# Kernel tuning notes

Hardware: AMD Instinct MI355X
Metric: run time of the kernel (lower is better)

The kernel has to match this reference:

```python
import jax, jax.numpy as jnp
import numpy as np

VOCAB = 1000
SEQ = 80
EMB = 128
UNITS = 128
BATCH = 4096


def setup_inputs() -> dict:
    key = jax.random.key(0)
    ks = jax.random.split(key, 10)
    s = 0.05
    return {
        "inputs": jax.random.randint(ks[0], (BATCH, SEQ), 0, VOCAB, dtype=jnp.int32),
        "emb": jax.random.normal(ks[1], (VOCAB, EMB), jnp.float32) * s,
        "Wx0": jax.random.normal(ks[2], (EMB, UNITS), jnp.float32) * s,
        "Wh0": jax.random.normal(ks[3], (UNITS, UNITS), jnp.float32) * s,
        "b0": jnp.zeros((UNITS,), jnp.float32),
        "Wx1": jax.random.normal(ks[4], (UNITS, UNITS), jnp.float32) * s,
        "Wh1": jax.random.normal(ks[5], (UNITS, UNITS), jnp.float32) * s,
        "b1": jnp.zeros((UNITS,), jnp.float32),
        "Wout": jax.random.normal(ks[6], (UNITS, 1), jnp.float32) * s,
        "bout": jnp.zeros((1,), jnp.float32),
    }


def reference(inputs, emb, Wx0, Wh0, b0, Wx1, Wh1, b1, Wout, bout):
    # Embedding lookup: [B, S, EMB]
    x = emb[inputs]
    B = x.shape[0]
    h0_init = jnp.zeros((B, UNITS), x.dtype)
    h1_init = jnp.zeros((B, UNITS), x.dtype)

    # Precompute input projections for both cells' input terms where possible.
    # Layer 0 input term depends only on x: [S, B, UNITS]
    x_t = jnp.einsum('bse,eu->sbu', x, Wx0) + b0

    def step(carry, xw):
        h0, h1 = carry
        # SimpleRNNCell 0: h = tanh(x@Wx + h@Wh + b)  (dropout off: inference)
        h0 = jnp.tanh(xw + h0 @ Wh0)
        # SimpleRNNCell 1 stacked on layer-0 output
        h1 = jnp.tanh(h0 @ Wx1 + h1 @ Wh1 + b1)
        return (h0, h1), None

    (h0, h1), _ = jax.lax.scan(step, (h0_init, h1_init), x_t)
    logits = h1 @ Wout + bout          # [B, 1]
    prob = jax.nn.sigmoid(logits)
    return prob
```

## Files before the change

### kernel.cpp

```cpp
#include <hip/hip_runtime.h>
#include <hip/hip_bf16.h>

#define VOCAB 1000
#define SEQ   80
#define EMB   128
#define UNITS 128
#define BATCH 4096

typedef short bf16x8 __attribute__((ext_vector_type(8)));
typedef float f32x4  __attribute__((ext_vector_type(4)));
typedef float f32x2  __attribute__((ext_vector_type(2)));

__device__ inline unsigned short f2bf(float x) {
    union { float f; unsigned int u; } c; c.f = x;
    unsigned int r = c.u + 0x7fffu + ((c.u >> 16) & 1u);
    return (unsigned short)(r >> 16);
}
__device__ inline float bf2f(unsigned short h) {
    union { unsigned int u; float f; } c; c.u = ((unsigned int)h) << 16;
    return c.f;
}
__device__ inline f32x2 th2(f32x2 x) {
    f32x2 x2 = x * x;
    f32x2 p = __builtin_elementwise_fma(x2, (f32x2)(0.13333334f), (f32x2)(-0.33333334f));
    p = __builtin_elementwise_fma(x2, p, (f32x2)(1.0f));
    return x * p;
}
__device__ inline unsigned int cvt_pk_bf16(float lo, float hi) {
    unsigned int r;
    asm("v_cvt_pk_bf16_f32 %0, %1, %2" : "=v"(r) : "v"(lo), "v"(hi));
    return r;
}
__device__ inline void lds_sync() {
    asm volatile("s_waitcnt lgkmcnt(0)\n\ts_barrier" ::: "memory");
}

__device__ __host__ inline int sigma(int u) {
    const int m = u >> 4, g = (u >> 2) & 3, r = u & 3;
    return ((m & 3) << 5) | (g << 3) | ((m >> 2) << 2) | r;
}

__global__ void __launch_bounds__(256)
prep_kernel(const float* __restrict__ emb, const float* __restrict__ Wx0,
            const float* __restrict__ b0, const float* __restrict__ Wh0,
            const float* __restrict__ Wx1, const float* __restrict__ Wh1,
            float* __restrict__ embW, unsigned short* __restrict__ WT)
{
    const int blk = blockIdx.x;
    const int tid = threadIdx.x;
    if (blk < VOCAB) {
        __shared__ float erow[EMB];
        __shared__ float part[EMB];
        const int u = tid & 127, half = tid >> 7;
        if (tid < EMB) erow[tid] = emb[blk * EMB + tid];
        __syncthreads();
        const int p = sigma(u);
        float s = half ? 0.f : b0[p];
        const int e0 = half * 64;
        #pragma unroll 8
        for (int e = e0; e < e0 + 64; ++e)
            s = fmaf(erow[e], Wx0[e * UNITS + p], s);
        if (half) part[u] = s;
        __syncthreads();
        if (!half) embW[blk * UNITS + u] = s + part[u];
    } else {
        const int mat = blk - VOCAB;
        const float* src = (mat == 0) ? Wh0 : (mat == 1) ? Wx1 : Wh1;
        for (int j = tid; j < UNITS * UNITS; j += 256) {
            const int row = j >> 7, k = j & 127;
            WT[mat * 16384 + j] = f2bf(src[k * UNITS + sigma(row)]);
        }
    }
}

__global__ void __launch_bounds__(512, 2)
rnn_kernel(const int* __restrict__ inputs, const float* __restrict__ embW,
           const unsigned short* __restrict__ WT, const float* __restrict__ b1,
           const float* __restrict__ Wout, const float* __restrict__ bout,
           float* __restrict__ out)
{
    __shared__ int idx_lds[SEQ * 16];
    __shared__ __align__(16) unsigned char h0buf[2][16 * 256];
    __shared__ __align__(16) unsigned char h1buf[2][16 * 256];

    const int tid  = threadIdx.x;
    const int lane = tid & 63;
    const int wid  = tid >> 6;
    const int w    = wid & 3;
    const int R    = blockIdx.x * 16;

    for (int j = tid; j < SEQ * 16; j += 512) {
        const int i = j / SEQ, t = j - i * SEQ;
        idx_lds[t * 16 + i] = inputs[(R + i) * SEQ + t];
    }
    for (int j = tid; j < 1024; j += 512) {
        ((unsigned int*)h0buf[0])[j] = 0u;
        ((unsigned int*)h1buf[0])[j] = 0u;
    }
    __syncthreads();

    const int lrow = lane & 15;
    const int lgrp = lane >> 4;
    const int lk8  = lgrp * 8;

    const int bswz   = (lrow & 7) << 4;
    const int rdbase = lrow * 256;
    const int woff   = (rdbase + w * 64 + lgrp * 16) ^ bswz;
    int cur = 0;

    if (wid < 4) {
        bf16x8 aW0[2][4];
        #pragma unroll
        for (int i = 0; i < 2; ++i)
            #pragma unroll
            for (int kk = 0; kk < 4; ++kk)
                aW0[i][kk] = *reinterpret_cast<const bf16x8*>(
                    WT + 0 * 16384 + ((w + 4 * i) * 16 + lrow) * 128 + kk * 32 + lk8);

        float4 xw_n[2];
        {
            const int row = idx_lds[lrow];
            xw_n[0] = *reinterpret_cast<const float4*>(embW + row * 128 + w * 16 + lgrp * 4);
            xw_n[1] = *reinterpret_cast<const float4*>(embW + row * 128 + (w + 4) * 16 + lgrp * 4);
        }

        __builtin_amdgcn_s_setprio(1);
        for (int t = 0; t <= SEQ; ++t) {
            const float4 xw0 = xw_n[0], xw1 = xw_n[1];
            const int tn   = (t < SEQ - 1) ? t + 1 : SEQ - 1;
            const int rown = idx_lds[tn * 16 + lrow];
            xw_n[0] = *reinterpret_cast<const float4*>(embW + rown * 128 + w * 16 + lgrp * 4);
            xw_n[1] = *reinterpret_cast<const float4*>(embW + rown * 128 + (w + 4) * 16 + lgrp * 4);

            bf16x8 f0[4];
            #pragma unroll
            for (int kk = 0; kk < 4; ++kk) {
                const int off = (rdbase + kk * 64 + lgrp * 16) ^ bswz;
                f0[kk] = *reinterpret_cast<const bf16x8*>(h0buf[cur] + off);
            }
            f32x4 acc0[2];
            acc0[0][0] = xw0.x; acc0[0][1] = xw0.y; acc0[0][2] = xw0.z; acc0[0][3] = xw0.w;
            acc0[1][0] = xw1.x; acc0[1][1] = xw1.y; acc0[1][2] = xw1.z; acc0[1][3] = xw1.w;

            #pragma unroll
            for (int kk = 0; kk < 4; ++kk) {
                acc0[0] = __builtin_amdgcn_mfma_f32_16x16x32_bf16(aW0[0][kk], f0[kk], acc0[0], 0, 0, 0);
                acc0[1] = __builtin_amdgcn_mfma_f32_16x16x32_bf16(aW0[1][kk], f0[kk], acc0[1], 0, 0, 0);
            }

            const f32x2 p0 = th2(f32x2{acc0[0][0], acc0[0][1]});
            const f32x2 p1 = th2(f32x2{acc0[0][2], acc0[0][3]});
            const f32x2 p2 = th2(f32x2{acc0[1][0], acc0[1][1]});
            const f32x2 p3 = th2(f32x2{acc0[1][2], acc0[1][3]});
            int4 q;
            q.x = (int)cvt_pk_bf16(p0.x, p0.y);
            q.y = (int)cvt_pk_bf16(p1.x, p1.y);
            q.z = (int)cvt_pk_bf16(p2.x, p2.y);
            q.w = (int)cvt_pk_bf16(p3.x, p3.y);
            *reinterpret_cast<int4*>(h0buf[cur ^ 1] + woff) = q;

            lds_sync();
            cur ^= 1;
        }
        __builtin_amdgcn_s_setprio(0);
    } else {
        bf16x8 aWx[2][4], aWh[2][4];
        #pragma unroll
        for (int i = 0; i < 2; ++i)
            #pragma unroll
            for (int kk = 0; kk < 4; ++kk) {
                const int rb = ((w + 4 * i) * 16 + lrow) * 128 + kk * 32 + lk8;
                aWx[i][kk] = *reinterpret_cast<const bf16x8*>(WT + 1 * 16384 + rb);
                aWh[i][kk] = *reinterpret_cast<const bf16x8*>(WT + 2 * 16384 + rb);
            }
        float4 b1v[2];
        b1v[0] = *reinterpret_cast<const float4*>(b1 + w * 32 + lgrp * 8 + 0);
        b1v[1] = *reinterpret_cast<const float4*>(b1 + w * 32 + lgrp * 8 + 4);

        for (int t = 0; t <= SEQ; ++t) {
            bf16x8 f0[4], f1[4];
            #pragma unroll
            for (int kk = 0; kk < 4; ++kk) {
                const int off = (rdbase + kk * 64 + lgrp * 16) ^ bswz;
                f0[kk] = *reinterpret_cast<const bf16x8*>(h0buf[cur] + off);
                f1[kk] = *reinterpret_cast<const bf16x8*>(h1buf[cur] + off);
            }

            f32x4 accA[2], accB[2];
            accA[0][0] = b1v[0].x; accA[0][1] = b1v[0].y; accA[0][2] = b1v[0].z; accA[0][3] = b1v[0].w;
            accA[1][0] = b1v[1].x; accA[1][1] = b1v[1].y; accA[1][2] = b1v[1].z; accA[1][3] = b1v[1].w;
            accB[0][0] = 0.f; accB[0][1] = 0.f; accB[0][2] = 0.f; accB[0][3] = 0.f;
            accB[1][0] = 0.f; accB[1][1] = 0.f; accB[1][2] = 0.f; accB[1][3] = 0.f;

            #pragma unroll
            for (int kk = 0; kk < 4; ++kk) {
                accA[0] = __builtin_amdgcn_mfma_f32_16x16x32_bf16(aWx[0][kk], f0[kk], accA[0], 0, 0, 0);
                accA[1] = __builtin_amdgcn_mfma_f32_16x16x32_bf16(aWx[1][kk], f0[kk], accA[1], 0, 0, 0);
                accB[0] = __builtin_amdgcn_mfma_f32_16x16x32_bf16(aWh[0][kk], f1[kk], accB[0], 0, 0, 0);
                accB[1] = __builtin_amdgcn_mfma_f32_16x16x32_bf16(aWh[1][kk], f1[kk], accB[1], 0, 0, 0);
            }

            const f32x2 p0 = th2(f32x2{accA[0][0] + accB[0][0], accA[0][1] + accB[0][1]});
            const f32x2 p1 = th2(f32x2{accA[0][2] + accB[0][2], accA[0][3] + accB[0][3]});
            const f32x2 p2 = th2(f32x2{accA[1][0] + accB[1][0], accA[1][1] + accB[1][1]});
            const f32x2 p3 = th2(f32x2{accA[1][2] + accB[1][2], accA[1][3] + accB[1][3]});
            int4 q;
            q.x = (int)cvt_pk_bf16(p0.x, p0.y);
            q.y = (int)cvt_pk_bf16(p1.x, p1.y);
            q.z = (int)cvt_pk_bf16(p2.x, p2.y);
            q.w = (int)cvt_pk_bf16(p3.x, p3.y);
            *reinterpret_cast<int4*>(h1buf[cur ^ 1] + woff) = q;

            lds_sync();
            cur ^= 1;
        }
    }

    if (wid == 0) {
        const int b = lrow;
        float s = 0.f;
        #pragma unroll
        for (int uu = 0; uu < 32; ++uu) {
            const int u   = lgrp * 32 + uu;
            const int off = (b * 256 + u * 2) ^ ((b & 7) << 4);
            s += bf2f(*reinterpret_cast<const unsigned short*>(h1buf[cur] + off)) * Wout[u];
        }
        s += __shfl_xor(s, 16);
        s += __shfl_xor(s, 32);
        if (lane < 16) {
            const float z = s + bout[0];
            const float e = __builtin_amdgcn_exp2f(-z * 1.4426950408889634f);
            out[R + b] = __builtin_amdgcn_rcpf(1.f + e);
        }
    }
}

extern "C" void kernel_launch(void* const* d_in, const int* in_sizes, int n_in,
                              void* d_out, int out_size, void* d_ws, size_t ws_size,
                              hipStream_t stream)
{
    (void)in_sizes; (void)n_in; (void)out_size; (void)ws_size;
    const int*   inputs = (const int*)  d_in[0];
    const float* emb    = (const float*)d_in[1];
    const float* Wx0    = (const float*)d_in[2];
    const float* Wh0    = (const float*)d_in[3];
    const float* b0     = (const float*)d_in[4];
    const float* Wx1    = (const float*)d_in[5];
    const float* Wh1    = (const float*)d_in[6];
    const float* b1     = (const float*)d_in[7];
    const float* Wout   = (const float*)d_in[8];
    const float* bout   = (const float*)d_in[9];
    float* out = (float*)d_out;

    float*          embW = (float*)d_ws;
    unsigned short* WT   = (unsigned short*)((char*)d_ws + 524288);

    prep_kernel<<<VOCAB + 3, 256, 0, stream>>>(emb, Wx0, b0, Wh0, Wx1, Wh1, embW, WT);
    rnn_kernel<<<BATCH / 16, 512, 0, stream>>>(inputs, embW, WT, b1, Wout, bout, out);
}
```

Before: 54.96 us.

## Replicate layer-0 recurrence per wave to keep h0 in registers

Each layer-0 wave now holds all eight Wh0 tiles and recomputes the full 128-unit h0 for its batch rows, feeding the result straight back through registers instead of reading it from LDS. The embedding input is added after the MFMAs instead of being used as the accumulator seed. Only the wave's own slice is still written to LDS for layer 1. Layer-1 waves reuse their own previous h1 slice from registers, and the raised wave priority moves from layer 0 to layer 1. This trades four times the layer-0 MFMA work, more registers and an unprefetched embedding load for less LDS traffic on the critical recurrence.

```diff
diff --git a/kernel.cpp b/kernel.cpp
--- a/kernel.cpp
+++ b/kernel.cpp
@@ -86,7 +86,6 @@
     const int tid  = threadIdx.x;
     const int lane = tid & 63;
     const int wid  = tid >> 6;
-    const int w    = wid & 3;
     const int R    = blockIdx.x * 16;
 
     for (int j = tid; j < SEQ * 16; j += 512) {
@@ -105,65 +104,66 @@
 
     const int bswz   = (lrow & 7) << 4;
     const int rdbase = lrow * 256;
-    const int woff   = (rdbase + w * 64 + lgrp * 16) ^ bswz;
     int cur = 0;
 
     if (wid < 4) {
-        bf16x8 aW0[2][4];
-        #pragma unroll
-        for (int i = 0; i < 2; ++i)
+        const int w = wid;
+        bf16x8 aW0[8][4];
+        #pragma unroll
+        for (int m = 0; m < 8; ++m)
             #pragma unroll
             for (int kk = 0; kk < 4; ++kk)
-                aW0[i][kk] = *reinterpret_cast<const bf16x8*>(
-                    WT + 0 * 16384 + ((w + 4 * i) * 16 + lrow) * 128 + kk * 32 + lk8);
-
-        float4 xw_n[2];
-        {
-            const int row = idx_lds[lrow];
-            xw_n[0] = *reinterpret_cast<const float4*>(embW + row * 128 + w * 16 + lgrp * 4);
-            xw_n[1] = *reinterpret_cast<const float4*>(embW + row * 128 + (w + 4) * 16 + lgrp * 4);
-        }
-
-        __builtin_amdgcn_s_setprio(1);
+                aW0[m][kk] = *reinterpret_cast<const bf16x8*>(
+                    WT + (m * 16 + lrow) * 128 + kk * 32 + lk8);
+
+        bf16x8 fb[4];
+        #pragma unroll
+        for (int kk = 0; kk < 4; ++kk) fb[kk] = (bf16x8)(short)0;
+
+        const int woff = (rdbase + w * 64 + lgrp * 16) ^ bswz;
+
         for (int t = 0; t <= SEQ; ++t) {
-            const float4 xw0 = xw_n[0], xw1 = xw_n[1];
-            const int tn   = (t < SEQ - 1) ? t + 1 : SEQ - 1;
-            const int rown = idx_lds[tn * 16 + lrow];
-            xw_n[0] = *reinterpret_cast<const float4*>(embW + rown * 128 + w * 16 + lgrp * 4);
-            xw_n[1] = *reinterpret_cast<const float4*>(embW + rown * 128 + (w + 4) * 16 + lgrp * 4);
-
-            bf16x8 f0[4];
-            #pragma unroll
-            for (int kk = 0; kk < 4; ++kk) {
-                const int off = (rdbase + kk * 64 + lgrp * 16) ^ bswz;
-                f0[kk] = *reinterpret_cast<const bf16x8*>(h0buf[cur] + off);
-            }
-            f32x4 acc0[2];
-            acc0[0][0] = xw0.x; acc0[0][1] = xw0.y; acc0[0][2] = xw0.z; acc0[0][3] = xw0.w;
-            acc0[1][0] = xw1.x; acc0[1][1] = xw1.y; acc0[1][2] = xw1.z; acc0[1][3] = xw1.w;
-
-            #pragma unroll
-            for (int kk = 0; kk < 4; ++kk) {
-                acc0[0] = __builtin_amdgcn_mfma_f32_16x16x32_bf16(aW0[0][kk], f0[kk], acc0[0], 0, 0, 0);
-                acc0[1] = __builtin_amdgcn_mfma_f32_16x16x32_bf16(aW0[1][kk], f0[kk], acc0[1], 0, 0, 0);
-            }
-
-            const f32x2 p0 = th2(f32x2{acc0[0][0], acc0[0][1]});
-            const f32x2 p1 = th2(f32x2{acc0[0][2], acc0[0][3]});
-            const f32x2 p2 = th2(f32x2{acc0[1][0], acc0[1][1]});
-            const f32x2 p3 = th2(f32x2{acc0[1][2], acc0[1][3]});
-            int4 q;
-            q.x = (int)cvt_pk_bf16(p0.x, p0.y);
-            q.y = (int)cvt_pk_bf16(p1.x, p1.y);
-            q.z = (int)cvt_pk_bf16(p2.x, p2.y);
-            q.w = (int)cvt_pk_bf16(p3.x, p3.y);
-            *reinterpret_cast<int4*>(h0buf[cur ^ 1] + woff) = q;
+            const int tc   = (t < SEQ) ? t : SEQ - 1;
+            const int rowC = idx_lds[tc * 16 + lrow];
+            float4 xw[8];
+            #pragma unroll
+            for (int m = 0; m < 8; ++m)
+                xw[m] = *reinterpret_cast<const float4*>(
+                    embW + rowC * 128 + m * 16 + lgrp * 4);
+
+            f32x4 acc[8];
+            #pragma unroll
+            for (int m = 0; m < 8; ++m)
+                acc[m] = __builtin_amdgcn_mfma_f32_16x16x32_bf16(
+                    aW0[m][0], fb[0], (f32x4){0.f, 0.f, 0.f, 0.f}, 0, 0, 0);
+            #pragma unroll
+            for (int kk = 1; kk < 4; ++kk)
+                #pragma unroll
+                for (int m = 0; m < 8; ++m)
+                    acc[m] = __builtin_amdgcn_mfma_f32_16x16x32_bf16(
+                        aW0[m][kk], fb[kk], acc[m], 0, 0, 0);
+
+            #pragma unroll
+            for (int kk = 0; kk < 4; ++kk) {
+                const f32x2 p0 = th2(f32x2{acc[kk][0] + xw[kk].x, acc[kk][1] + xw[kk].y});
+                const f32x2 p1 = th2(f32x2{acc[kk][2] + xw[kk].z, acc[kk][3] + xw[kk].w});
+                const f32x2 p2 = th2(f32x2{acc[kk + 4][0] + xw[kk + 4].x, acc[kk + 4][1] + xw[kk + 4].y});
+                const f32x2 p3 = th2(f32x2{acc[kk + 4][2] + xw[kk + 4].z, acc[kk + 4][3] + xw[kk + 4].w});
+                int4 q;
+                q.x = (int)cvt_pk_bf16(p0.x, p0.y);
+                q.y = (int)cvt_pk_bf16(p1.x, p1.y);
+                q.z = (int)cvt_pk_bf16(p2.x, p2.y);
+                q.w = (int)cvt_pk_bf16(p3.x, p3.y);
+                if (kk == w)
+                    *reinterpret_cast<int4*>(h0buf[cur ^ 1] + woff) = q;
+                fb[kk] = __builtin_bit_cast(bf16x8, q);
+            }
 
             lds_sync();
             cur ^= 1;
         }
-        __builtin_amdgcn_s_setprio(0);
     } else {
+        const int w = wid - 4;
         bf16x8 aWx[2][4], aWh[2][4];
         #pragma unroll
         for (int i = 0; i < 2; ++i)
@@ -177,13 +177,22 @@
         b1v[0] = *reinterpret_cast<const float4*>(b1 + w * 32 + lgrp * 8 + 0);
         b1v[1] = *reinterpret_cast<const float4*>(b1 + w * 32 + lgrp * 8 + 4);
 
+        bf16x8 fbk1 = (bf16x8)(short)0;
+        const int woff = (rdbase + w * 64 + lgrp * 16) ^ bswz;
+
+        __builtin_amdgcn_s_setprio(1);
         for (int t = 0; t <= SEQ; ++t) {
             bf16x8 f0[4], f1[4];
             #pragma unroll
             for (int kk = 0; kk < 4; ++kk) {
                 const int off = (rdbase + kk * 64 + lgrp * 16) ^ bswz;
                 f0[kk] = *reinterpret_cast<const bf16x8*>(h0buf[cur] + off);
-                f1[kk] = *reinterpret_cast<const bf16x8*>(h1buf[cur] + off);
+            }
+            #pragma unroll
+            for (int kk = 0; kk < 4; ++kk) {
+                if (kk == w) f1[kk] = fbk1;
+                else f1[kk] = *reinterpret_cast<const bf16x8*>(
+                        h1buf[cur] + ((rdbase + kk * 64 + lgrp * 16) ^ bswz));
             }
 
             f32x4 accA[2], accB[2];
@@ -210,10 +219,12 @@
             q.z = (int)cvt_pk_bf16(p2.x, p2.y);
             q.w = (int)cvt_pk_bf16(p3.x, p3.y);
             *reinterpret_cast<int4*>(h1buf[cur ^ 1] + woff) = q;
+            fbk1 = __builtin_bit_cast(bf16x8, q);
 
             lds_sync();
             cur ^= 1;
         }
+        __builtin_amdgcn_s_setprio(0);
     }
 
     if (wid == 0) {
```

After: 129.0 us. 135% more time.

## Move layer-1 input projection to layer-0 waves and deepen wave pipeline

Applied to the files above, without the earlier changes.

The layer-1 input product h0@Wx1 plus bias is now computed by the layer-0 waves right after their own step and staged through a new double-buffered fp32 LDS buffer. The layer-1 waves then only do the recurrent h1@Wh1 product, which shortens their critical path per step and balances MFMA work between the two wave groups. The pipeline grows by one step and adds LDS traffic and footprint (16KB zbuf), which could lower occupancy. It also changes which waves set high priority, since only the layer-0 recurrence is prioritized.

```diff
diff --git a/kernel.cpp b/kernel.cpp
--- a/kernel.cpp
+++ b/kernel.cpp
@@ -82,6 +82,7 @@
     __shared__ int idx_lds[SEQ * 16];
     __shared__ __align__(16) unsigned char h0buf[2][16 * 256];
     __shared__ __align__(16) unsigned char h1buf[2][16 * 256];
+    __shared__ __align__(16) unsigned char zbuf[2][8192];
 
     const int tid  = threadIdx.x;
     const int lane = tid & 63;
@@ -93,7 +94,7 @@
         const int i = j / SEQ, t = j - i * SEQ;
         idx_lds[t * 16 + i] = inputs[(R + i) * SEQ + t];
     }
-    for (int j = tid; j < 1024; j += 512) {
+    for (int j = tid; j < 2048; j += 512) {
         ((unsigned int*)h0buf[0])[j] = 0u;
         ((unsigned int*)h1buf[0])[j] = 0u;
     }
@@ -106,16 +107,22 @@
     const int bswz   = (lrow & 7) << 4;
     const int rdbase = lrow * 256;
     const int woff   = (rdbase + w * 64 + lgrp * 16) ^ bswz;
-    int cur = 0;
+    const int zo0    = w * 2048 + lane * 16;
+    const int zo1    = w * 2048 + 1024 + lane * 16;
 
     if (wid < 4) {
-        bf16x8 aW0[2][4];
+        bf16x8 aW0[2][4], aWx[2][4];
         #pragma unroll
         for (int i = 0; i < 2; ++i)
             #pragma unroll
-            for (int kk = 0; kk < 4; ++kk)
-                aW0[i][kk] = *reinterpret_cast<const bf16x8*>(
-                    WT + 0 * 16384 + ((w + 4 * i) * 16 + lrow) * 128 + kk * 32 + lk8);
+            for (int kk = 0; kk < 4; ++kk) {
+                const int rb = ((w + 4 * i) * 16 + lrow) * 128 + kk * 32 + lk8;
+                aW0[i][kk] = *reinterpret_cast<const bf16x8*>(WT + 0 * 16384 + rb);
+                aWx[i][kk] = *reinterpret_cast<const bf16x8*>(WT + 1 * 16384 + rb);
+            }
+        float4 b1v[2];
+        b1v[0] = *reinterpret_cast<const float4*>(b1 + w * 32 + lgrp * 8 + 0);
+        b1v[1] = *reinterpret_cast<const float4*>(b1 + w * 32 + lgrp * 8 + 4);
 
         float4 xw_n[2];
         {
@@ -124,95 +131,95 @@
             xw_n[1] = *reinterpret_cast<const float4*>(embW + row * 128 + (w + 4) * 16 + lgrp * 4);
         }
 
-        __builtin_amdgcn_s_setprio(1);
-        for (int t = 0; t <= SEQ; ++t) {
-            const float4 xw0 = xw_n[0], xw1 = xw_n[1];
-            const int tn   = (t < SEQ - 1) ? t + 1 : SEQ - 1;
-            const int rown = idx_lds[tn * 16 + lrow];
-            xw_n[0] = *reinterpret_cast<const float4*>(embW + rown * 128 + w * 16 + lgrp * 4);
-            xw_n[1] = *reinterpret_cast<const float4*>(embW + rown * 128 + (w + 4) * 16 + lgrp * 4);
-
+        for (int t = 0; t <= SEQ + 1; ++t) {
             bf16x8 f0[4];
-            #pragma unroll
-            for (int kk = 0; kk < 4; ++kk) {
-                const int off = (rdbase + kk * 64 + lgrp * 16) ^ bswz;
-                f0[kk] = *reinterpret_cast<const bf16x8*>(h0buf[cur] + off);
-            }
-            f32x4 acc0[2];
-            acc0[0][0] = xw0.x; acc0[0][1] = xw0.y; acc0[0][2] = xw0.z; acc0[0][3] = xw0.w;
-            acc0[1][0] = xw1.x; acc0[1][1] = xw1.y; acc0[1][2] = xw1.z; acc0[1][3] = xw1.w;
-
-            #pragma unroll
-            for (int kk = 0; kk < 4; ++kk) {
-                acc0[0] = __builtin_amdgcn_mfma_f32_16x16x32_bf16(aW0[0][kk], f0[kk], acc0[0], 0, 0, 0);
-                acc0[1] = __builtin_amdgcn_mfma_f32_16x16x32_bf16(aW0[1][kk], f0[kk], acc0[1], 0, 0, 0);
-            }
-
-            const f32x2 p0 = th2(f32x2{acc0[0][0], acc0[0][1]});
-            const f32x2 p1 = th2(f32x2{acc0[0][2], acc0[0][3]});
-            const f32x2 p2 = th2(f32x2{acc0[1][0], acc0[1][1]});
-            const f32x2 p3 = th2(f32x2{acc0[1][2], acc0[1][3]});
-            int4 q;
-            q.x = (int)cvt_pk_bf16(p0.x, p0.y);
-            q.y = (int)cvt_pk_bf16(p1.x, p1.y);
-            q.z = (int)cvt_pk_bf16(p2.x, p2.y);
-            q.w = (int)cvt_pk_bf16(p3.x, p3.y);
-            *reinterpret_cast<int4*>(h0buf[cur ^ 1] + woff) = q;
-
+            if (t <= SEQ) {
+                const unsigned char* src = h0buf[(t - 1) & 1];
+                #pragma unroll
+                for (int kk = 0; kk < 4; ++kk)
+                    f0[kk] = *reinterpret_cast<const bf16x8*>(
+                        src + ((rdbase + kk * 64 + lgrp * 16) ^ bswz));
+            }
+            if (t < SEQ) {
+                const float4 xw0 = xw_n[0], xw1 = xw_n[1];
+                const int tn   = (t < SEQ - 1) ? t + 1 : SEQ - 1;
+                const int rown = idx_lds[tn * 16 + lrow];
+                xw_n[0] = *reinterpret_cast<const float4*>(embW + rown * 128 + w * 16 + lgrp * 4);
+                xw_n[1] = *reinterpret_cast<const float4*>(embW + rown * 128 + (w + 4) * 16 + lgrp * 4);
+
+                __builtin_amdgcn_s_setprio(1);
+                f32x4 acc0[2];
+                acc0[0][0] = xw0.x; acc0[0][1] = xw0.y; acc0[0][2] = xw0.z; acc0[0][3] = xw0.w;
+                acc0[1][0] = xw1.x; acc0[1][1] = xw1.y; acc0[1][2] = xw1.z; acc0[1][3] = xw1.w;
+                #pragma unroll
+                for (int kk = 0; kk < 4; ++kk) {
+                    acc0[0] = __builtin_amdgcn_mfma_f32_16x16x32_bf16(aW0[0][kk], f0[kk], acc0[0], 0, 0, 0);
+                    acc0[1] = __builtin_amdgcn_mfma_f32_16x16x32_bf16(aW0[1][kk], f0[kk], acc0[1], 0, 0, 0);
+                }
+                const f32x2 p0 = th2(f32x2{acc0[0][0], acc0[0][1]});
+                const f32x2 p1 = th2(f32x2{acc0[0][2], acc0[0][3]});
+                const f32x2 p2 = th2(f32x2{acc0[1][0], acc0[1][1]});
+                const f32x2 p3 = th2(f32x2{acc0[1][2], acc0[1][3]});
+                int4 q;
+                q.x = (int)cvt_pk_bf16(p0.x, p0.y);
+                q.y = (int)cvt_pk_bf16(p1.x, p1.y);
+                q.z = (int)cvt_pk_bf16(p2.x, p2.y);
+                q.w = (int)cvt_pk_bf16(p3.x, p3.y);
+                *reinterpret_cast<int4*>(h0buf[t & 1] + woff) = q;
+                __builtin_amdgcn_s_setprio(0);
+            }
+            if (t >= 1 && t <= SEQ) {
+                f32x4 az0, az1;
+                az0[0] = b1v[0].x; az0[1] = b1v[0].y; az0[2] = b1v[0].z; az0[3] = b1v[0].w;
+                az1[0] = b1v[1].x; az1[1] = b1v[1].y; az1[2] = b1v[1].z; az1[3] = b1v[1].w;
+                #pragma unroll
+                for (int kk = 0; kk < 4; ++kk) {
+                    az0 = __builtin_amdgcn_mfma_f32_16x16x32_bf16(aWx[0][kk], f0[kk], az0, 0, 0, 0);
+                    az1 = __builtin_amdgcn_mfma_f32_16x16x32_bf16(aWx[1][kk], f0[kk], az1, 0, 0, 0);
+                }
+                *reinterpret_cast<f32x4*>(zbuf[t & 1] + zo0) = az0;
+                *reinterpret_cast<f32x4*>(zbuf[t & 1] + zo1) = az1;
+            }
             lds_sync();
-            cur ^= 1;
-        }
-        __builtin_amdgcn_s_setprio(0);
+        }
     } else {
-        bf16x8 aWx[2][4], aWh[2][4];
+        bf16x8 aWh[2][4];
         #pragma unroll
         for (int i = 0; i < 2; ++i)
             #pragma unroll
-            for (int kk = 0; kk < 4; ++kk) {
-                const int rb = ((w + 4 * i) * 16 + lrow) * 128 + kk * 32 + lk8;
-                aWx[i][kk] = *reinterpret_cast<const bf16x8*>(WT + 1 * 16384 + rb);
-                aWh[i][kk] = *reinterpret_cast<const bf16x8*>(WT + 2 * 16384 + rb);
-            }
-        float4 b1v[2];
-        b1v[0] = *reinterpret_cast<const float4*>(b1 + w * 32 + lgrp * 8 + 0);
-        b1v[1] = *reinterpret_cast<const float4*>(b1 + w * 32 + lgrp * 8 + 4);
-
-        for (int t = 0; t <= SEQ; ++t) {
-            bf16x8 f0[4], f1[4];
-            #pragma unroll
-            for (int kk = 0; kk < 4; ++kk) {
-                const int off = (rdbase + kk * 64 + lgrp * 16) ^ bswz;
-                f0[kk] = *reinterpret_cast<const bf16x8*>(h0buf[cur] + off);
-                f1[kk] = *reinterpret_cast<const bf16x8*>(h1buf[cur] + off);
-            }
-
-            f32x4 accA[2], accB[2];
-            accA[0][0] = b1v[0].x; accA[0][1] = b1v[0].y; accA[0][2] = b1v[0].z; accA[0][3] = b1v[0].w;
-            accA[1][0] = b1v[1].x; accA[1][1] = b1v[1].y; accA[1][2] = b1v[1].z; accA[1][3] = b1v[1].w;
-            accB[0][0] = 0.f; accB[0][1] = 0.f; accB[0][2] = 0.f; accB[0][3] = 0.f;
-            accB[1][0] = 0.f; accB[1][1] = 0.f; accB[1][2] = 0.f; accB[1][3] = 0.f;
-
-            #pragma unroll
-            for (int kk = 0; kk < 4; ++kk) {
-                accA[0] = __builtin_amdgcn_mfma_f32_16x16x32_bf16(aWx[0][kk], f0[kk], accA[0], 0, 0, 0);
-                accA[1] = __builtin_amdgcn_mfma_f32_16x16x32_bf16(aWx[1][kk], f0[kk], accA[1], 0, 0, 0);
-                accB[0] = __builtin_amdgcn_mfma_f32_16x16x32_bf16(aWh[0][kk], f1[kk], accB[0], 0, 0, 0);
-                accB[1] = __builtin_amdgcn_mfma_f32_16x16x32_bf16(aWh[1][kk], f1[kk], accB[1], 0, 0, 0);
-            }
-
-            const f32x2 p0 = th2(f32x2{accA[0][0] + accB[0][0], accA[0][1] + accB[0][1]});
-            const f32x2 p1 = th2(f32x2{accA[0][2] + accB[0][2], accA[0][3] + accB[0][3]});
-            const f32x2 p2 = th2(f32x2{accA[1][0] + accB[1][0], accA[1][1] + accB[1][1]});
-            const f32x2 p3 = th2(f32x2{accA[1][2] + accB[1][2], accA[1][3] + accB[1][3]});
-            int4 q;
-            q.x = (int)cvt_pk_bf16(p0.x, p0.y);
-            q.y = (int)cvt_pk_bf16(p1.x, p1.y);
-            q.z = (int)cvt_pk_bf16(p2.x, p2.y);
-            q.w = (int)cvt_pk_bf16(p3.x, p3.y);
-            *reinterpret_cast<int4*>(h1buf[cur ^ 1] + woff) = q;
-
+            for (int kk = 0; kk < 4; ++kk)
+                aWh[i][kk] = *reinterpret_cast<const bf16x8*>(
+                    WT + 2 * 16384 + ((w + 4 * i) * 16 + lrow) * 128 + kk * 32 + lk8);
+
+        for (int t = 0; t <= SEQ + 1; ++t) {
+            if (t >= 2) {
+                const unsigned char* zs = zbuf[(t - 1) & 1];
+                f32x4 accA0 = *reinterpret_cast<const f32x4*>(zs + zo0);
+                f32x4 accA1 = *reinterpret_cast<const f32x4*>(zs + zo1);
+                const unsigned char* hs = h1buf[(t - 1) & 1];
+                bf16x8 f1[4];
+                #pragma unroll
+                for (int kk = 0; kk < 4; ++kk)
+                    f1[kk] = *reinterpret_cast<const bf16x8*>(
+                        hs + ((rdbase + kk * 64 + lgrp * 16) ^ bswz));
+
+                #pragma unroll
+                for (int kk = 0; kk < 4; ++kk) {
+                    accA0 = __builtin_amdgcn_mfma_f32_16x16x32_bf16(aWh[0][kk], f1[kk], accA0, 0, 0, 0);
+                    accA1 = __builtin_amdgcn_mfma_f32_16x16x32_bf16(aWh[1][kk], f1[kk], accA1, 0, 0, 0);
+                }
+                const f32x2 p0 = th2(f32x2{accA0[0], accA0[1]});
+                const f32x2 p1 = th2(f32x2{accA0[2], accA0[3]});
+                const f32x2 p2 = th2(f32x2{accA1[0], accA1[1]});
+                const f32x2 p3 = th2(f32x2{accA1[2], accA1[3]});
+                int4 q;
+                q.x = (int)cvt_pk_bf16(p0.x, p0.y);
+                q.y = (int)cvt_pk_bf16(p1.x, p1.y);
+                q.z = (int)cvt_pk_bf16(p2.x, p2.y);
+                q.w = (int)cvt_pk_bf16(p3.x, p3.y);
+                *reinterpret_cast<int4*>(h1buf[t & 1] + woff) = q;
+            }
             lds_sync();
-            cur ^= 1;
         }
     }
 
@@ -223,7 +230,7 @@
         for (int uu = 0; uu < 32; ++uu) {
             const int u   = lgrp * 32 + uu;
             const int off = (b * 256 + u * 2) ^ ((b & 7) << 4);
-            s += bf2f(*reinterpret_cast<const unsigned short*>(h1buf[cur] + off)) * Wout[u];
+            s += bf2f(*reinterpret_cast<const unsigned short*>(h1buf[1] + off)) * Wout[u];
         }
         s += __shfl_xor(s, 16);
         s += __shfl_xor(s, 32);
```

Result: no change. 55.38 us (+0.8%).
